# Performance work log

Hardware: AMD Instinct MI355X
Metric: run time of the kernel (lower is better)

## Reference

```python
import jax, jax.numpy as jnp
import numpy as np
import math
from itertools import permutations

B, C_IN, C_OUT, K, N, D, F_DIM = 2, 4, 8, 4, 224, 2, 128


def _make_perms(k):
    # [k!, k, k] permutation matrices, same ordering as itertools.permutations
    nP = math.factorial(k)
    perms = np.zeros((nP, k, k), dtype=np.float32)
    for c, p in enumerate(permutations(range(k))):
        perms[c, np.arange(k), np.array(p)] = 1.0
    return jnp.asarray(perms)


def setup_inputs() -> dict:
    key = jax.random.key(0)
    ks = jax.random.split(key, 6)
    graph = jax.random.normal(ks[0], (B, C_IN, N, N), jnp.float32)
    types = jax.random.normal(ks[1], (B, C_IN, N), jnp.float32)
    features = jax.random.normal(ks[2], (B, N, F_DIM), jnp.float32)
    # xavier-uniform-ish scales for the learned kernels
    k_struct = jax.random.normal(ks[3], (C_OUT, C_IN, K, K), jnp.float32) * 0.3
    k_row = jax.random.normal(ks[4], (C_OUT, C_IN, K), jnp.float32) * 0.5
    k_col = jax.random.normal(ks[5], (C_OUT, C_IN, K), jnp.float32) * 0.5
    return {"graph": graph, "types": types, "features": features,
            "k_struct": k_struct, "k_row": k_row, "k_col": k_col}


def _forward(graph, types, features, k_struct, k_row, k_col):
    Bn, C, Nn, _ = graph.shape
    k = k_struct.shape[-1]
    new_k = (k - 1) * D + 1
    nH = Nn - new_k + 1            # square graph -> nW == nH
    n_sub = nH * nH
    idx = jnp.arange(nH)[:, None] + jnp.arange(k) * D  # [nH, k] dilated window indices

    # --- _prepare: dilated subgraph extraction (vectorized gather) ---
    g = graph[:, :, idx, :]            # [B,C,nH,k,N]
    g = g[..., idx]                    # [B,C,nH,k,nH,k]
    sub = jnp.transpose(g, (0, 2, 4, 1, 3, 5)).reshape(Bn, n_sub, C, k, k)
    rt = jnp.transpose(types[:, :, idx], (0, 2, 1, 3))  # [B,nH,C,k]
    row_t = jnp.broadcast_to(rt[:, :, None], (Bn, nH, nH, C, k)).reshape(Bn, n_sub, C, k)
    col_t = jnp.broadcast_to(rt[:, None, :], (Bn, nH, nH, C, k)).reshape(Bn, n_sub, C, k)
    rf = features[:, idx, :].sum(axis=-2)              # [B,nH,F]
    feats = rf[:, :, None, :] + rf[:, None, :, :]      # row_features + col_features
    h_mean = feats.reshape(Bn, n_sub, -1).mean(axis=1)  # [B,F]

    # --- permuted kernels ---
    perms = _make_perms(k)                                  # [P,k,k]
    Kp = jnp.einsum('pau,oiuv,pbv->oipab', perms, k_struct, perms)  # P K P^T
    Rp = jnp.einsum('pau,oiu->oipa', perms, k_row)
    Cp = jnp.einsum('pau,oiu->oipa', perms, k_col)

    subf = sub.reshape(-1, C, k, k)   # [n,i,a,b], n = B*n_sub
    rtf = row_t.reshape(-1, C, k)
    ctf = col_t.reshape(-1, C, k)

    # ||X - Y||_F^2 = ||X||^2 + ||Y||^2 - 2<X,Y>, avoids the huge broadcasted diff
    def sq_dist(x2_ni, y2_opi, cross_nopi):
        return y2_opi[None] + x2_ni[:, None, None, :] - 2.0 * cross_nopi

    G2 = jnp.sum(subf * subf, axis=(-2, -1))                       # [n,i]
    K2 = jnp.transpose(jnp.sum(Kp * Kp, axis=(-2, -1)), (0, 2, 1))  # [o,p,i]
    struct = sq_dist(G2, K2, jnp.einsum('niab,oipab->nopi', subf, Kp))
    R2 = jnp.transpose(jnp.sum(Rp * Rp, axis=-1), (0, 2, 1))
    rsim = sq_dist(jnp.sum(rtf * rtf, axis=-1), R2, jnp.einsum('nia,oipa->nopi', rtf, Rp))
    C2 = jnp.transpose(jnp.sum(Cp * Cp, axis=-1), (0, 2, 1))
    csim = sq_dist(jnp.sum(ctf * ctf, axis=-1), C2, jnp.einsum('nia,oipa->nopi', ctf, Cp))

    total = struct + rsim + csim            # [n, o, P, i]
    # maxpool over P of (-total), negated back == min over permutations of total
    pooled = jnp.min(total, axis=2)         # [n, o, i]
    sims = jnp.transpose(pooled.reshape(Bn, n_sub, -1), (0, 2, 1))  # [B, o*i, n_sub]
    out_sim = (1.0 - jax.nn.softmax(sims, axis=-1)) / sims.shape[-1]
    return h_mean, out_sim


def reference(graph, types, features, k_struct, k_row, k_col):
    return _forward(graph, types, features, k_struct, k_row, k_col)
```

## Files before the change

### kernel.cpp

```cpp
#include <hip/hip_runtime.h>
#include <hip/hip_bf16.h>

#define B_    2
#define CIN   4
#define COUT  8
#define KK    4
#define DD    2
#define NN    224
#define FDIM  128
#define NH    218
#define NSUB  (NH*NH)
#define NPERM 24
#define NROWS (B_*COUT*CIN)
#define NSUB4 (NSUB/4)
#define CH4   512
#define MB    ((NSUB4 + CH4 - 1) / CH4)
#define OG    2
#define NCHUNK ((NSUB + 255) / 256)
#define NEGBIG (-3.4e38f)

__device__ static constexpr int PERM[NPERM][4] = {
  {0,1,2,3},{0,1,3,2},{0,2,1,3},{0,2,3,1},{0,3,1,2},{0,3,2,1},
  {1,0,2,3},{1,0,3,2},{1,2,0,3},{1,2,3,0},{1,3,0,2},{1,3,2,0},
  {2,0,1,3},{2,0,3,1},{2,1,0,3},{2,1,3,0},{2,3,0,1},{2,3,1,0},
  {3,0,1,2},{3,0,2,1},{3,1,0,2},{3,1,2,0},{3,2,0,1},{3,2,1,0}
};

__global__ __launch_bounds__(64) void hmean_kernel(const float* __restrict__ features,
                                                   float* __restrict__ out) {
  int bf = blockIdx.x;
  int b = bf / FDIM, f = bf - b * FDIM;
  int lane = threadIdx.x;
  const float* fb = features + (size_t)b * NN * FDIM + f;
  float acc = 0.f;
  for (int r = lane; r < NN; r += 64) {
    int w = 0;
#pragma unroll
    for (int a = 0; a < KK; ++a) {
      int i0 = r - a * DD;
      if (0 <= i0 && i0 < NH) w++;
    }
    acc += (float)w * fb[(size_t)r * FDIM];
  }
#pragma unroll
  for (int off = 32; off > 0; off >>= 1) acc += __shfl_down(acc, off, 64);
  if (lane == 0) out[bf] = acc * (2.0f / (float)NH);
}

__global__ __launch_bounds__(256) void sims_kernel(
    const float* __restrict__ graph, const float* __restrict__ types,
    const float* __restrict__ ksA, const float* __restrict__ krA,
    const float* __restrict__ kcA, float* __restrict__ simsOut,
    float* __restrict__ partial)
{
  __shared__ float ls[COUT * CIN * 16];
  __shared__ float lr[COUT * CIN * 4];
  __shared__ float lc[COUT * CIN * 4];
  __shared__ float lK2[COUT * CIN];
  __shared__ float red[4 * 4];
  int t = threadIdx.x;
  for (int i = t; i < COUT * CIN * 16; i += 256) ls[i] = ksA[i];
  for (int i = t; i < COUT * CIN * 4; i += 256) { lr[i] = krA[i]; lc[i] = kcA[i]; }
  __syncthreads();
  if (t < COUT * CIN) {
    float k2 = 0.f;
#pragma unroll
    for (int u = 0; u < 16; ++u) k2 += ls[t * 16 + u] * ls[t * 16 + u];
#pragma unroll
    for (int u = 0; u < 4; ++u) k2 += lr[t * 4 + u] * lr[t * 4 + u] + lc[t * 4 + u] * lc[t * 4 + u];
    lK2[t] = k2;
  }
  __syncthreads();

  int s_raw = blockIdx.x * 256 + t;
  bool valid = (s_raw < NSUB);
  int s = valid ? s_raw : (NSUB - 1);
  int yi  = blockIdx.y;
  int og  = yi >> 3;
  int bci = yi & 7;
  int b   = bci >> 2;
  int ci  = bci & 3;
  int ii  = s / NH;
  int jj  = s - ii * NH;

  const float* gi = graph + ((size_t)b * CIN + ci) * NN * NN;
  const float* ti = types + ((size_t)b * CIN + ci) * NN;

  float subv[16], rtv[4], ctv[4];
  float G2 = 0.f, T2r = 0.f, T2c = 0.f;
#pragma unroll
  for (int a = 0; a < KK; ++a) {
    const float* row = gi + (size_t)(ii + a * DD) * NN + jj;
#pragma unroll
    for (int bb = 0; bb < KK; ++bb) {
      float v = row[bb * DD];
      subv[a * 4 + bb] = v;
      G2 += v * v;
    }
    float rv = ti[ii + a * DD];
    float cv = ti[jj + a * DD];
    rtv[a] = rv; ctv[a] = cv;
    T2r += rv * rv; T2c += cv * cv;
  }
  float base0 = G2 + T2r + T2c;

  int wave = t >> 6, lane = t & 63;

#pragma unroll 1
  for (int oo = 0; oo < COUT / OG; ++oo) {
    int o = og * (COUT / OG) + oo;
    int oc = o * CIN + ci;
    const float* pS = ls + oc * 16;
    const float* pR = lr + oc * 4;
    const float* pC = lc + oc * 4;
    float kS[16], kR[4], kC[4];
#pragma unroll
    for (int u = 0; u < 16; ++u) kS[u] = pS[u];
#pragma unroll
    for (int u = 0; u < 4; ++u) { kR[u] = pR[u]; kC[u] = pC[u]; }

    float C1[16];
#pragma unroll
    for (int a = 0; a < 4; ++a)
#pragma unroll
      for (int ap = 0; ap < 4; ++ap)
        C1[a * 4 + ap] = subv[a * 4 + a] * kS[ap * 4 + ap]
                       + rtv[a] * kR[ap] + ctv[a] * kC[ap];

    float maxcr = NEGBIG;
#pragma unroll
    for (int p = 0; p < NPERM; ++p) {
      const int p0 = PERM[p][0], p1 = PERM[p][1], p2 = PERM[p][2], p3 = PERM[p][3];
      float cr = C1[0 * 4 + p0] + C1[1 * 4 + p1] + C1[2 * 4 + p2] + C1[3 * 4 + p3];
      cr += subv[0*4+1] * kS[p0*4+p1];
      cr += subv[0*4+2] * kS[p0*4+p2];
      cr += subv[0*4+3] * kS[p0*4+p3];
      cr += subv[1*4+0] * kS[p1*4+p0];
      cr += subv[1*4+2] * kS[p1*4+p2];
      cr += subv[1*4+3] * kS[p1*4+p3];
      cr += subv[2*4+0] * kS[p2*4+p0];
      cr += subv[2*4+1] * kS[p2*4+p1];
      cr += subv[2*4+3] * kS[p2*4+p3];
      cr += subv[3*4+0] * kS[p3*4+p0];
      cr += subv[3*4+1] * kS[p3*4+p1];
      cr += subv[3*4+2] * kS[p3*4+p2];
      maxcr = fmaxf(maxcr, cr);
    }
    float best = base0 + lK2[oc] - 2.0f * maxcr;
    if (valid)
      simsOut[(((size_t)b * COUT + o) * CIN + ci) * NSUB + s] = best;

    float bm = valid ? best : NEGBIG;
    float m = bm;
#pragma unroll
    for (int off = 32; off > 0; off >>= 1) m = fmaxf(m, __shfl_down(m, off, 64));
    if (lane == 0) red[wave] = m;
    __syncthreads();
    float m_blk = fmaxf(fmaxf(red[0], red[1]), fmaxf(red[2], red[3]));
    float e = valid ? __expf(bm - m_blk) : 0.f;
#pragma unroll
    for (int off = 32; off > 0; off >>= 1) e += __shfl_down(e, off, 64);
    __syncthreads();
    if (lane == 0) red[4 + wave] = e;
    __syncthreads();
    if (t == 0) {
      float l_blk = red[4] + red[5] + red[6] + red[7];
      int rowc = (((b * COUT + o) * CIN + ci) * NCHUNK + blockIdx.x) * 2;
      partial[rowc]     = m_blk;
      partial[rowc + 1] = l_blk;
    }
    __syncthreads();
  }
}

__global__ __launch_bounds__(256) void softmax_combine(const float* __restrict__ partial,
                                                       float* __restrict__ stats) {
  int row = blockIdx.x;
  int t = threadIdx.x;
  float m = NEGBIG, l = 0.f;
  if (t < NCHUNK) {
    m = partial[(row * NCHUNK + t) * 2];
    l = partial[(row * NCHUNK + t) * 2 + 1];
  }
  __shared__ float ms[256], lsum[256];
  ms[t] = m; lsum[t] = l;
  __syncthreads();
  for (int off = 128; off > 0; off >>= 1) {
    if (t < off) {
      float m2 = ms[t + off], l2 = lsum[t + off];
      float M = fmaxf(ms[t], m2);
      lsum[t] = lsum[t] * __expf(ms[t] - M) + l2 * __expf(m2 - M);
      ms[t] = M;
    }
    __syncthreads();
  }
  if (t == 0) { stats[2 * row] = ms[0]; stats[2 * row + 1] = 1.0f / lsum[0]; }
}

__global__ __launch_bounds__(256) void softmax_final(float* __restrict__ sims,
                                                     const float* __restrict__ stats) {
  int blk = blockIdx.x;
  int row = blk / MB;
  int ch  = blk - row * MB;
  int base4 = ch * CH4;
  int n4 = NSUB4 - base4; if (n4 > CH4) n4 = CH4;
  float4* rp = (float4*)(sims + (size_t)row * NSUB) + base4;
  float M = stats[2 * row], invS = stats[2 * row + 1];
  const float scale = 1.0f / (float)NSUB;
  for (int i = threadIdx.x; i < n4; i += 256) {
    float4 v = rp[i];
    v.x = (1.0f - __expf(v.x - M) * invS) * scale;
    v.y = (1.0f - __expf(v.y - M) * invS) * scale;
    v.z = (1.0f - __expf(v.z - M) * invS) * scale;
    v.w = (1.0f - __expf(v.w - M) * invS) * scale;
    rp[i] = v;
  }
}

extern "C" void kernel_launch(void* const* d_in, const int* in_sizes, int n_in,
                              void* d_out, int out_size, void* d_ws, size_t ws_size,
                              hipStream_t stream) {
  const float* graph    = (const float*)d_in[0];
  const float* types    = (const float*)d_in[1];
  const float* features = (const float*)d_in[2];
  const float* ks       = (const float*)d_in[3];
  const float* kr       = (const float*)d_in[4];
  const float* kc       = (const float*)d_in[5];
  float* out  = (float*)d_out;
  float* sims = out + B_ * FDIM;

  float* partial = (float*)d_ws;
  float* stats   = partial + NROWS * NCHUNK * 2;

  hmean_kernel<<<B_ * FDIM, 64, 0, stream>>>(features, out);
  dim3 sgrid(NCHUNK, B_ * CIN * OG);
  sims_kernel<<<sgrid, 256, 0, stream>>>(graph, types, ks, kr, kc, sims, partial);
  softmax_combine<<<NROWS, 256, 0, stream>>>(partial, stats);
  softmax_final<<<NROWS * MB, 256, 0, stream>>>(sims, stats);
}
```

Before: 122.0 us.

## Process two subgraphs per thread with packed float2 math and per-wave softmax partials

Each thread now handles two subgraph positions using 2-wide float vectors, so the permutation inner loop can map to packed FMA instructions and each kernel value loaded from LDS is reused twice. The block-level softmax reduction with several __syncthreads is replaced by per-wave partial (max, sum) values written to the workspace. The combine kernel is changed to fold a larger number of partials per row. This halves the grid, doubles register pressure per thread, and moves more reduction work into the combine step.

Result: faster. 108.2 us (-11.3%).

```diff
diff --git a/kernel.cpp b/kernel.cpp
--- a/kernel.cpp
+++ b/kernel.cpp
@@ -16,8 +16,11 @@
 #define CH4   512
 #define MB    ((NSUB4 + CH4 - 1) / CH4)
 #define OG    2
-#define NCHUNK ((NSUB + 255) / 256)
+#define NCH2  ((NSUB + 511) / 512)
+#define NW    4
 #define NEGBIG (-3.4e38f)
+
+typedef float v2f __attribute__((ext_vector_type(2)));
 
 __device__ static constexpr int PERM[NPERM][4] = {
   {0,1,2,3},{0,1,3,2},{0,2,1,3},{0,2,3,1},{0,3,1,2},{0,3,2,1},
@@ -57,7 +60,6 @@
   __shared__ float lr[COUT * CIN * 4];
   __shared__ float lc[COUT * CIN * 4];
   __shared__ float lK2[COUT * CIN];
-  __shared__ float red[4 * 4];
   int t = threadIdx.x;
   for (int i = t; i < COUT * CIN * 16; i += 256) ls[i] = ksA[i];
   for (int i = t; i < COUT * CIN * 4; i += 256) { lr[i] = krA[i]; lc[i] = kcA[i]; }
@@ -72,37 +74,40 @@
   }
   __syncthreads();
 
-  int s_raw = blockIdx.x * 256 + t;
-  bool valid = (s_raw < NSUB);
-  int s = valid ? s_raw : (NSUB - 1);
+  int s0r = blockIdx.x * 512 + t;
+  int s1r = s0r + 256;
+  bool v0 = (s0r < NSUB), v1 = (s1r < NSUB);
+  int s0 = v0 ? s0r : (NSUB - 1);
+  int s1 = v1 ? s1r : (NSUB - 1);
   int yi  = blockIdx.y;
   int og  = yi >> 3;
   int bci = yi & 7;
   int b   = bci >> 2;
   int ci  = bci & 3;
-  int ii  = s / NH;
-  int jj  = s - ii * NH;
+  int ii0 = s0 / NH, jj0 = s0 - ii0 * NH;
+  int ii1 = s1 / NH, jj1 = s1 - ii1 * NH;
 
   const float* gi = graph + ((size_t)b * CIN + ci) * NN * NN;
   const float* ti = types + ((size_t)b * CIN + ci) * NN;
 
-  float subv[16], rtv[4], ctv[4];
-  float G2 = 0.f, T2r = 0.f, T2c = 0.f;
+  v2f subv[16], rtv[4], ctv[4];
+  v2f G2 = 0.f, T2r = 0.f, T2c = 0.f;
 #pragma unroll
   for (int a = 0; a < KK; ++a) {
-    const float* row = gi + (size_t)(ii + a * DD) * NN + jj;
+    const float* r0 = gi + (size_t)(ii0 + a * DD) * NN + jj0;
+    const float* r1 = gi + (size_t)(ii1 + a * DD) * NN + jj1;
 #pragma unroll
     for (int bb = 0; bb < KK; ++bb) {
-      float v = row[bb * DD];
+      v2f v; v.x = r0[bb * DD]; v.y = r1[bb * DD];
       subv[a * 4 + bb] = v;
       G2 += v * v;
     }
-    float rv = ti[ii + a * DD];
-    float cv = ti[jj + a * DD];
+    v2f rv; rv.x = ti[ii0 + a * DD]; rv.y = ti[ii1 + a * DD];
+    v2f cv; cv.x = ti[jj0 + a * DD]; cv.y = ti[jj1 + a * DD];
     rtv[a] = rv; ctv[a] = cv;
     T2r += rv * rv; T2c += cv * cv;
   }
-  float base0 = G2 + T2r + T2c;
+  v2f base0 = G2 + T2r + T2c;
 
   int wave = t >> 6, lane = t & 63;
 
@@ -110,16 +115,21 @@
   for (int oo = 0; oo < COUT / OG; ++oo) {
     int o = og * (COUT / OG) + oo;
     int oc = o * CIN + ci;
-    const float* pS = ls + oc * 16;
-    const float* pR = lr + oc * 4;
-    const float* pC = lc + oc * 4;
     float kS[16], kR[4], kC[4];
-#pragma unroll
-    for (int u = 0; u < 16; ++u) kS[u] = pS[u];
-#pragma unroll
-    for (int u = 0; u < 4; ++u) { kR[u] = pR[u]; kC[u] = pC[u]; }
-
-    float C1[16];
+    {
+      const float4* pS4 = (const float4*)(ls + oc * 16);
+#pragma unroll
+      for (int u = 0; u < 4; ++u) {
+        float4 q = pS4[u];
+        kS[u*4+0] = q.x; kS[u*4+1] = q.y; kS[u*4+2] = q.z; kS[u*4+3] = q.w;
+      }
+      float4 qr = *(const float4*)(lr + oc * 4);
+      kR[0] = qr.x; kR[1] = qr.y; kR[2] = qr.z; kR[3] = qr.w;
+      float4 qc = *(const float4*)(lc + oc * 4);
+      kC[0] = qc.x; kC[1] = qc.y; kC[2] = qc.z; kC[3] = qc.w;
+    }
+
+    v2f C1[16];
 #pragma unroll
     for (int a = 0; a < 4; ++a)
 #pragma unroll
@@ -127,11 +137,11 @@
         C1[a * 4 + ap] = subv[a * 4 + a] * kS[ap * 4 + ap]
                        + rtv[a] * kR[ap] + ctv[a] * kC[ap];
 
-    float maxcr = NEGBIG;
+    v2f maxcr = NEGBIG;
 #pragma unroll
     for (int p = 0; p < NPERM; ++p) {
       const int p0 = PERM[p][0], p1 = PERM[p][1], p2 = PERM[p][2], p3 = PERM[p][3];
-      float cr = C1[0 * 4 + p0] + C1[1 * 4 + p1] + C1[2 * 4 + p2] + C1[3 * 4 + p3];
+      v2f cr = C1[0 * 4 + p0] + C1[1 * 4 + p1] + C1[2 * 4 + p2] + C1[3 * 4 + p3];
       cr += subv[0*4+1] * kS[p0*4+p1];
       cr += subv[0*4+2] * kS[p0*4+p2];
       cr += subv[0*4+3] * kS[p0*4+p3];
@@ -144,32 +154,30 @@
       cr += subv[3*4+0] * kS[p3*4+p0];
       cr += subv[3*4+1] * kS[p3*4+p1];
       cr += subv[3*4+2] * kS[p3*4+p2];
-      maxcr = fmaxf(maxcr, cr);
-    }
-    float best = base0 + lK2[oc] - 2.0f * maxcr;
-    if (valid)
-      simsOut[(((size_t)b * COUT + o) * CIN + ci) * NSUB + s] = best;
-
-    float bm = valid ? best : NEGBIG;
-    float m = bm;
+      maxcr = __builtin_elementwise_max(maxcr, cr);
+    }
+    v2f best = base0 + lK2[oc] - 2.0f * maxcr;
+
+    int rowIdx = (b * COUT + o) * CIN + ci;
+    size_t rowbase = (size_t)rowIdx * NSUB;
+    if (v0) simsOut[rowbase + s0r] = best.x;
+    if (v1) simsOut[rowbase + s1r] = best.y;
+
+    float bm0 = v0 ? best.x : NEGBIG;
+    float bm1 = v1 ? best.y : NEGBIG;
+    float m = fmaxf(bm0, bm1);
 #pragma unroll
     for (int off = 32; off > 0; off >>= 1) m = fmaxf(m, __shfl_down(m, off, 64));
-    if (lane == 0) red[wave] = m;
-    __syncthreads();
-    float m_blk = fmaxf(fmaxf(red[0], red[1]), fmaxf(red[2], red[3]));
-    float e = valid ? __expf(bm - m_blk) : 0.f;
+    m = __shfl(m, 0, 64);
+    float e = 0.f;
+    if (v0) e += __expf(bm0 - m);
+    if (v1) e += __expf(bm1 - m);
 #pragma unroll
     for (int off = 32; off > 0; off >>= 1) e += __shfl_down(e, off, 64);
-    __syncthreads();
-    if (lane == 0) red[4 + wave] = e;
-    __syncthreads();
-    if (t == 0) {
-      float l_blk = red[4] + red[5] + red[6] + red[7];
-      int rowc = (((b * COUT + o) * CIN + ci) * NCHUNK + blockIdx.x) * 2;
-      partial[rowc]     = m_blk;
-      partial[rowc + 1] = l_blk;
-    }
-    __syncthreads();
+    if (lane == 0) {
+      int idx = ((rowIdx * NCH2 + blockIdx.x) * NW + wave) * 2;
+      partial[idx] = m; partial[idx + 1] = e;
+    }
   }
 }
 
@@ -177,24 +185,27 @@
                                                        float* __restrict__ stats) {
   int row = blockIdx.x;
   int t = threadIdx.x;
+  const float* pp = partial + (size_t)row * NCH2 * NW * 2;
   float m = NEGBIG, l = 0.f;
-  if (t < NCHUNK) {
-    m = partial[(row * NCHUNK + t) * 2];
-    l = partial[(row * NCHUNK + t) * 2 + 1];
-  }
-  __shared__ float ms[256], lsum[256];
-  ms[t] = m; lsum[t] = l;
+  for (int i = t; i < NCH2 * NW; i += 256) {
+    float mi = pp[2 * i], li = pp[2 * i + 1];
+    float M = fmaxf(m, mi);
+    l = l * __expf(m - M) + li * __expf(mi - M);
+    m = M;
+  }
+  __shared__ float ms[256], lsv[256];
+  ms[t] = m; lsv[t] = l;
   __syncthreads();
   for (int off = 128; off > 0; off >>= 1) {
     if (t < off) {
-      float m2 = ms[t + off], l2 = lsum[t + off];
+      float m2 = ms[t + off], l2 = lsv[t + off];
       float M = fmaxf(ms[t], m2);
-      lsum[t] = lsum[t] * __expf(ms[t] - M) + l2 * __expf(m2 - M);
+      lsv[t] = lsv[t] * __expf(ms[t] - M) + l2 * __expf(m2 - M);
       ms[t] = M;
     }
     __syncthreads();
   }
-  if (t == 0) { stats[2 * row] = ms[0]; stats[2 * row + 1] = 1.0f / lsum[0]; }
+  if (t == 0) { stats[2 * row] = ms[0]; stats[2 * row + 1] = 1.0f / lsv[0]; }
 }
 
 __global__ __launch_bounds__(256) void softmax_final(float* __restrict__ sims,
@@ -230,10 +241,10 @@
   float* sims = out + B_ * FDIM;
 
   float* partial = (float*)d_ws;
-  float* stats   = partial + NROWS * NCHUNK * 2;
+  float* stats   = partial + NROWS * NCH2 * NW * 2;
 
   hmean_kernel<<<B_ * FDIM, 64, 0, stream>>>(features, out);
-  dim3 sgrid(NCHUNK, B_ * CIN * OG);
+  dim3 sgrid(NCH2, B_ * CIN * OG);
   sims_kernel<<<sgrid, 256, 0, stream>>>(graph, types, ks, kr, kc, sims, partial);
   softmax_combine<<<NROWS, 256, 0, stream>>>(partial, stats);
   softmax_final<<<NROWS * MB, 256, 0, stream>>>(sims, stats);
```
